# Optimization experiments

Hardware: AMD Instinct MI355X
Metric: run time of the kernel (lower is better)

## Reference

```python
import jax, jax.numpy as jnp
import numpy as np

EPS = 0.5
MU = 1.0
N_CLASS = 10
N = 131072
D = 128


def setup_inputs() -> dict:
    key = jax.random.key(0)
    k1, k2, k3 = jax.random.split(key, 3)
    Z = jax.random.normal(k1, (N, D), dtype=jnp.float32)
    labels = jax.random.randint(k2, (N,), 0, N_CLASS)
    Pi = jax.nn.one_hot(labels, N_CLASS, dtype=jnp.float32)  # [N, C] membership
    Us = jax.random.normal(k3, (N_CLASS, D, D), dtype=jnp.float32)
    return {"Z": Z, "Pi": Pi, "Us": Us}


def reference(Z, Pi, Us):
    # Z: [n, d]; forward uses Zt = Z.T of shape [d, n]
    n, d = Z.shape
    nf = jnp.asarray(n, Z.dtype)
    df = jnp.asarray(d, Z.dtype)
    I = jnp.eye(d, dtype=Z.dtype)

    # --- loss_discrimn: 0.5 * logdet(I + d/(n*eps) * Zt @ Zt.T), Zt@Zt.T = Z.T@Z ([d,d])
    gram = Z.T @ Z
    sign, logabsdet = jnp.linalg.slogdet(I + (df / (nf * EPS)) * gram)
    loss_R = 0.5 * logabsdet

    # --- loss_compress: per-class log of squared column norms of Us[j]
    trPi = Pi.sum(axis=0)                      # [C]
    col_norms_sq = (Us ** 2).sum(axis=1)       # [C, d] (norm over rows = axis 0 of Us[j])
    per_class = jnp.log1p((df / (trPi[:, None] * EPS)) * col_norms_sq).sum(axis=1)  # [C]
    loss_Rc = ((trPi / (2.0 * nf)) * per_class).sum()

    # --- reg_U: sum_j || Z.T @ diag(Pi_j) @ Z - Us[j] Us[j].T ||_F^2
    # column-scaled contraction instead of materializing n x n diag
    M = jnp.einsum('nd,nj,ne->jde', Z, Pi, Z)      # [C, d, d]
    UUt = jnp.einsum('jdk,jek->jde', Us, Us)       # [C, d, d]
    loss_reg = 0.5 * MU * ((M - UUt) ** 2).sum()

    loss_obj = loss_R - loss_Rc - loss_reg
    return (-loss_obj, loss_R, loss_Rc, loss_reg)
```

## Files before the change

kernel.cpp:

```cpp
#include <hip/hip_runtime.h>
#include <hip/hip_bf16.h>

#define DD 128
#define NCLS 10
#define CHUNK 512
#define KSTEP 32

typedef __attribute__((ext_vector_type(8))) short s16x8;
typedef __attribute__((ext_vector_type(4))) float f32x4;
typedef __attribute__((ext_vector_type(4))) unsigned int u32x4;
typedef __attribute__((ext_vector_type(8))) unsigned short u16x8;
typedef __attribute__((ext_vector_type(4))) unsigned short u16x4;

union FU { unsigned u[4]; s16x8 v; };

__device__ inline unsigned short f2bf(float x) {
  union { float f; unsigned u; } c; c.f = x;
  unsigned u = c.u;
  u += 0x7fffu + ((u >> 16) & 1u);
  return (unsigned short)(u >> 16);
}

__device__ __forceinline__ void frags4(const char* lds, int g, int m, int c0, FU* F) {
  const char* fb = lds + g * (4 * 528) + m * 4;
#pragma unroll
  for (int ft = 0; ft < 4; ft++) {
    const char* p = fb + (c0 + ft * 16) * 4;
    F[ft].u[0] = *(const unsigned*)(p);
    F[ft].u[1] = *(const unsigned*)(p + 528);
    F[ft].u[2] = *(const unsigned*)(p + 1056);
    F[ft].u[3] = *(const unsigned*)(p + 1584);
  }
}

__global__ void k_init(int* __restrict__ ws32) {
  ws32[threadIdx.x] = 0;
}

__global__ void k_label(const float* __restrict__ Pi, int N, int nbk,
                        unsigned char* __restrict__ label, int* __restrict__ meta) {
  __shared__ float pish[2560];
  __shared__ int h[NCLS];
  int t = threadIdx.x;
  if (t < NCLS) h[t] = 0;
  size_t base4 = (size_t)blockIdx.x * 640;
  size_t tot4 = (size_t)N * NCLS / 4;
  {
    const f32x4* src = (const f32x4*)Pi;
    f32x4* dst = (f32x4*)pish;
    for (int i = t; i < 640; i += 256) {
      size_t gi = base4 + i;
      f32x4 z = {0.f, 0.f, 0.f, 0.f};
      dst[i] = (gi < tot4) ? src[gi] : z;
    }
  }
  __syncthreads();
  int n = blockIdx.x * 256 + t;
  if (n < N) {
    const float* p = &pish[t * NCLS];
    float best = p[0]; int bj = 0;
#pragma unroll
    for (int j = 1; j < NCLS; j++) { float v = p[j]; if (v > best) { best = v; bj = j; } }
    label[n] = (unsigned char)bj;
    atomicAdd(&h[bj], 1);
  }
  __syncthreads();
  if (t < NCLS) {
    atomicAdd(&meta[t], h[t]);
    __threadfence();
  }
  __syncthreads();
  if (t == 0) {
    int done = atomicAdd(&meta[63], 1);
    if (done == nbk - 1) {
      int cs = 0;
      meta[10] = 0;
#pragma unroll
      for (int j = 0; j < NCLS; j++) {
        int cnt = atomicAdd(&meta[j], 0);
        int cp = (cnt + CHUNK - 1) / CHUNK;
        meta[32 + j] = cs * CHUNK;
        cs += cp;
        meta[10 + j + 1] = cs;
      }
      __threadfence();
    }
  }
}

__global__ __launch_bounds__(256) void k_pack(const float* __restrict__ Z,
                                              const float* __restrict__ Us,
                                              const unsigned char* __restrict__ label,
                                              int* __restrict__ meta,
                                              float* __restrict__ scal,
                                              unsigned short* __restrict__ packed,
                                              float* __restrict__ UUt,
                                              float nf, int nb) {
  __shared__ __align__(16) char pool[9472];
  __shared__ int h[NCLS], loff[NCLS], gbase[NCLS];
  __shared__ int slotOf[256];
  __shared__ float fred[8];
  int b = blockIdx.x, t = threadIdx.x;

  if (b < nb) {
    size_t n0 = (size_t)b * 256;
    if (t < NCLS) h[t] = 0;
    __syncthreads();
    int n = (int)n0 + t;
    int myj = 0, myr = 0;
    bool act = (n < (int)nf);
    if (act) { myj = label[n]; myr = atomicAdd(&h[myj], 1); }
    __syncthreads();
    if (t == 0) {
      int c = 0;
#pragma unroll
      for (int j = 0; j < NCLS; j++) { loff[j] = c; c += h[j]; }
    }
    __syncthreads();
    if (t < NCLS) gbase[t] = atomicAdd(&meta[32 + t], h[t]);
    __syncthreads();
    slotOf[t] = act ? (gbase[myj] + myr) : -1;
    __syncthreads();
    int rr = t >> 4, q = t & 15;
#pragma unroll 4
    for (int pass = 0; pass < 16; pass++) {
      int r = pass * 16 + rr;
      int dst = slotOf[r];
      if (dst < 0) continue;
      const float* zp = Z + (n0 + r) * DD + q * 8;
      f32x4 v0 = *(const f32x4*)zp;
      f32x4 v1 = *(const f32x4*)(zp + 4);
      u32x4 u;
      u[0] = (unsigned)f2bf(v0[0]) | ((unsigned)f2bf(v0[1]) << 16);
      u[1] = (unsigned)f2bf(v0[2]) | ((unsigned)f2bf(v0[3]) << 16);
      u[2] = (unsigned)f2bf(v1[0]) | ((unsigned)f2bf(v1[1]) << 16);
      u[3] = (unsigned)f2bf(v1[2]) | ((unsigned)f2bf(v1[3]) << 16);
      *(u32x4*)((char*)packed + (size_t)dst * 256 + q * 16) = u;
    }
  } else if (b < nb + NCLS) {
    int j = b - nb;
    int dstart = meta[10 + j] * CHUNK + meta[j];
    int dend = meta[11 + j] * CHUNK;
    int nrows = dend - dstart;
    u32x4 z = {0u, 0u, 0u, 0u};
    for (int i = t; i < nrows * 16; i += 256)
      *(u32x4*)((char*)packed + (size_t)dstart * 256 + (size_t)i * 16) = z;
  } else {
    int j = b - nb - NCLS;
    const float* U = Us + (size_t)j * 16384;
    {
      float* cs = (float*)(pool + 8448);
      float* red2 = (float*)(pool + 8960);
      int e = t & 127, half = t >> 7;
      float acc = 0.0f;
      int dd0 = half * 64;
      for (int d2 = dd0; d2 < dd0 + 64; d2++) { float v = U[d2 * 128 + e]; acc += v * v; }
      if (half == 0) cs[e] = acc;
      __syncthreads();
      float trj = (float)meta[j];
      float term = 0.0f;
      if (half == 1) {
        float tot = cs[e] + acc;
        term = log1pf((256.0f / trj) * tot);
      }
#pragma unroll
      for (int o = 32; o; o >>= 1) term += __shfl_down(term, o);
      if ((t & 63) == 0) red2[t >> 6] = term;
      __syncthreads();
      if (t == 0) atomicAdd(&scal[1], (trj / (2.0f * nf)) * (red2[2] + red2[3]));
    }
    __syncthreads();
    char* ldsY = pool;
    int l = t & 63, w = t >> 6;
    int g = l >> 4, m = l & 15;
    int d0 = (w >> 1) * 64, e0 = (w & 1) * 64;
    int sk2 = t >> 4, q = t & 15;
    f32x4 acc[4][4] = {};
    for (int ks = 0; ks < 4; ks++) {
      int k0 = ks * 32;
      __syncthreads();
      unsigned wv[8];
#pragma unroll
      for (int i = 0; i < 8; i++) {
        int c = 8 * q + i;
        wv[i] = (unsigned)f2bf(U[c * 128 + k0 + 2 * sk2])
              | ((unsigned)f2bf(U[c * 128 + k0 + 2 * sk2 + 1]) << 16);
      }
      u32x4 w0 = {wv[0], wv[1], wv[2], wv[3]};
      u32x4 w1 = {wv[4], wv[5], wv[6], wv[7]};
      *(u32x4*)(ldsY + sk2 * 528 + q * 32) = w0;
      *(u32x4*)(ldsY + sk2 * 528 + q * 32 + 16) = w1;
      __syncthreads();
      FU A[4], B[4];
      frags4(ldsY, g, m, d0, A);
      if (e0 != d0) frags4(ldsY, g, m, e0, B);
      else { for (int i = 0; i < 4; i++) B[i] = A[i]; }
#pragma unroll
      for (int dt = 0; dt < 4; dt++)
#pragma unroll
        for (int et = 0; et < 4; et++)
          acc[dt][et] = __builtin_amdgcn_mfma_f32_16x16x32_bf16(A[dt].v, B[et].v, acc[dt][et], 0, 0, 0);
    }
    float* uo = UUt + (size_t)j * 16384;
    float sq = 0.f;
#pragma unroll
    for (int dt = 0; dt < 4; dt++)
#pragma unroll
      for (int et = 0; et < 4; et++)
#pragma unroll
        for (int r = 0; r < 4; r++) {
          int row = d0 + dt * 16 + g * 4 + r;
          int col = e0 + et * 16 + m;
          float p = acc[dt][et][r];
          uo[row * 128 + col] = p;
          sq += p * p;
        }
#pragma unroll
    for (int o = 32; o; o >>= 1) sq += __shfl_down(sq, o);
    if (l == 0) fred[w] = sq;
    __syncthreads();
    if (t == 0) atomicAdd(&scal[2], fred[0] + fred[1] + fred[2] + fred[3]);
  }
}

__global__ __launch_bounds__(256, 2) void k_syrk(const unsigned short* __restrict__ packed,
                                                 const int* __restrict__ meta,
                                                 const float* __restrict__ UUt,
                                                 float* __restrict__ partial,
                                                 float* __restrict__ scal) {
  __shared__ __align__(16) char tilec[2][8448];
  __shared__ float tred[8];
  int b = blockIdx.x, t = threadIdx.x;
  if (b >= meta[20]) return;
  int l = t & 63, w = t >> 6;
  int g = l >> 4, m = l & 15;
  int d0 = (w >> 1) * 64, e0 = (w & 1) * 64;
  int sk2 = t >> 4, q = t & 15;
  size_t rowbase = (size_t)b * CHUNK;
  f32x4 acc[4][4] = {};

  auto PACKW = [&](const u16x8& a, const u16x8& bb, int buf) {
    unsigned wv[8];
#pragma unroll
    for (int i = 0; i < 8; i++)
      wv[i] = (unsigned)(unsigned short)a[i] | ((unsigned)(unsigned short)bb[i] << 16);
    u32x4 w0 = {wv[0], wv[1], wv[2], wv[3]};
    u32x4 w1 = {wv[4], wv[5], wv[6], wv[7]};
    char* tb = tilec[buf] + sk2 * 528 + q * 32;
    *(u32x4*)tb = w0;
    *(u32x4*)(tb + 16) = w1;
  };
  auto COMPUTE = [&](int buf) {
    FU A[4], B[4];
    frags4(tilec[buf], g, m, d0, A);
    if (d0 != e0) frags4(tilec[buf], g, m, e0, B);
    else { for (int i = 0; i < 4; i++) B[i] = A[i]; }
#pragma unroll
    for (int dt = 0; dt < 4; dt++)
#pragma unroll
      for (int et = 0; et < 4; et++)
        acc[dt][et] = __builtin_amdgcn_mfma_f32_16x16x32_bf16(A[dt].v, B[et].v, acc[dt][et], 0, 0, 0);
  };

  {
    const unsigned short* src = packed + rowbase * DD;
    u16x8 a = *(const u16x8*)(src + (2 * sk2) * DD + q * 8);
    u16x8 bb = *(const u16x8*)(src + (2 * sk2 + 1) * DD + q * 8);
    PACKW(a, bb, 0);
  }
  __syncthreads();
  for (int ks = 0; ks < CHUNK / KSTEP; ks++) {
    u16x8 na, nb2;
    bool more = (ks + 1 < CHUNK / KSTEP);
    if (more) {
      const unsigned short* src = packed + (rowbase + (size_t)(ks + 1) * KSTEP) * DD;
      na = *(const u16x8*)(src + (2 * sk2) * DD + q * 8);
      nb2 = *(const u16x8*)(src + (2 * sk2 + 1) * DD + q * 8);
    }
    COMPUTE(ks & 1);
    __syncthreads();
    if (more) PACKW(na, nb2, (ks + 1) & 1);
    __syncthreads();
  }

  int j = 0;
#pragma unroll
  for (int jj = 1; jj < NCLS; jj++) if (b >= meta[10 + jj]) j = jj;
  float* pb = partial + (size_t)b * 16384;
  const float* uu = UUt + (size_t)j * 16384;
  float trloc = 0.0f, dot = 0.0f;
#pragma unroll
  for (int dt = 0; dt < 4; dt++)
#pragma unroll
    for (int et = 0; et < 4; et++)
#pragma unroll
      for (int r = 0; r < 4; r++) {
        int row = d0 + dt * 16 + g * 4 + r;
        int col = e0 + et * 16 + m;
        float p = acc[dt][et][r];
        pb[row * 128 + col] = p;
        dot += p * uu[row * 128 + col];
        if (row == col) trloc += p;
      }
#pragma unroll
  for (int o = 32; o; o >>= 1) { trloc += __shfl_down(trloc, o); dot += __shfl_down(dot, o); }
  if (l == 0) { tred[w] = trloc; tred[4 + w] = dot; }
  __syncthreads();
  if (t == 0) {
    atomicAdd(&scal[0], tred[0] + tred[1] + tred[2] + tred[3]);
    atomicAdd(&scal[2], -2.0f * (tred[4] + tred[5] + tred[6] + tred[7]));
  }
}

__global__ void k_reduceE(const float* __restrict__ partial, const int* __restrict__ meta,
                          float* __restrict__ scal, float* __restrict__ E,
                          unsigned short* __restrict__ Ebf, float cf) {
  __shared__ float red[12];
  int t = threadIdx.x;
  int idx = blockIdx.x * 256 + t;
  float gsum = 0.f, sqs = 0.f;
#pragma unroll
  for (int j = 0; j < NCLS; j++) {
    int c0 = meta[10 + j], c1 = meta[11 + j];
    float s = 0.f;
#pragma unroll 4
    for (int c = c0; c < c1; c++) s += partial[(size_t)c * 16384 + idx];
    gsum += s; sqs += s * s;
  }
  float c = 1.0f + cf * scal[0] * (1.0f / 128.0f);
  float rc = 1.0f / c;
  int dg = ((idx >> 7) == (idx & 127)) ? 1 : 0;
  float e = (cf * rc) * gsum + (dg ? (rc - 1.0f) : 0.0f);
  E[idx] = e;
  Ebf[idx] = f2bf(e);
  float p1 = dg ? e : 0.0f;
  float p2 = e * e;
#pragma unroll
  for (int o = 32; o; o >>= 1) {
    p1 += __shfl_down(p1, o); p2 += __shfl_down(p2, o); sqs += __shfl_down(sqs, o);
  }
  if ((t & 63) == 0) { int wv = t >> 6; red[wv] = p1; red[4 + wv] = p2; red[8 + wv] = sqs; }
  __syncthreads();
  if (t == 0) {
    atomicAdd(&scal[3], red[0] + red[1] + red[2] + red[3]);
    atomicAdd(&scal[4], red[4] + red[5] + red[6] + red[7]);
    atomicAdd(&scal[2], red[8] + red[9] + red[10] + red[11]);
  }
}

__global__ __launch_bounds__(256) void k_final(const unsigned short* __restrict__ Ebf,
                                               const float* __restrict__ E,
                                               const float* __restrict__ scal,
                                               float* __restrict__ out, float cf) {
  __shared__ __align__(16) char ldsX[8448];
  __shared__ __align__(16) char ldsY[8448];
  __shared__ float red[4][4];
  int t = threadIdx.x;
  int l = t & 63, w = t >> 6;
  int g = l >> 4, m = l & 15;
  int d0 = (w >> 1) * 64, e0 = (w & 1) * 64;
  int sk2 = t >> 4, sq = t & 15;

  auto STAGE_X = [&](int ks) {
    int k0 = ks * 32 + 2 * sk2;
#pragma unroll
    for (int qi = 0; qi < 2; qi++) {
      int q = sq + qi * 16;
      u16x4 a = *(const u16x4*)(Ebf + k0 * 128 + q * 4);
      u16x4 bb = *(const u16x4*)(Ebf + (k0 + 1) * 128 + q * 4);
      u32x4 u;
#pragma unroll
      for (int i = 0; i < 4; i++) u[i] = (unsigned)a[i] | ((unsigned)bb[i] << 16);
      *(u32x4*)(ldsX + sk2 * 528 + q * 16) = u;
    }
  };

  f32x4 acc2[4][4] = {};
  for (int ks = 0; ks < 4; ks++) {
    __syncthreads();
    STAGE_X(ks);
    __syncthreads();
    FU A[4], B[4];
    frags4(ldsX, g, m, d0, A);
    if (e0 != d0) frags4(ldsX, g, m, e0, B);
    else { for (int i = 0; i < 4; i++) B[i] = A[i]; }
#pragma unroll
    for (int dt = 0; dt < 4; dt++)
#pragma unroll
      for (int et = 0; et < 4; et++)
        acc2[dt][et] = __builtin_amdgcn_mfma_f32_16x16x32_bf16(A[dt].v, B[et].v, acc2[dt][et], 0, 0, 0);
  }
  float t3 = 0.f, t4 = 0.f;
#pragma unroll
  for (int dt = 0; dt < 4; dt++)
#pragma unroll
    for (int et = 0; et < 4; et++)
#pragma unroll
      for (int r = 0; r < 4; r++) {
        int row = d0 + dt * 16 + g * 4 + r;
        int col = e0 + et * 16 + m;
        float p = acc2[dt][et][r];
        t3 += p * E[row * 128 + col];
        t4 += p * p;
      }

  f32x4 acc3[4][4] = {};
  for (int ks = 0; ks < 4; ks++) {
    __syncthreads();
    STAGE_X(ks);
    int dsrc = (ks < 2) ? 0 : 64;
    if (d0 == dsrc) {
      int dtb = 2 * (ks & 1);
#pragma unroll
      for (int dd = 0; dd < 2; dd++) {
        int dt = dtb + dd;
#pragma unroll
        for (int et = 0; et < 4; et++)
#pragma unroll
          for (int r = 0; r < 4; r++) {
            int lrow = dd * 16 + g * 4 + r;
            int col = e0 + et * 16 + m;
            unsigned short v = f2bf(acc2[dt][et][r]);
            *(unsigned short*)(ldsY + (lrow >> 1) * 528 + col * 4 + (lrow & 1) * 2) = v;
          }
      }
    }
    __syncthreads();
    FU A[4], B[4];
    frags4(ldsX, g, m, d0, A);
    frags4(ldsY, g, m, e0, B);
#pragma unroll
    for (int dt = 0; dt < 4; dt++)
#pragma unroll
      for (int et = 0; et < 4; et++)
        acc3[dt][et] = __builtin_amdgcn_mfma_f32_16x16x32_bf16(A[dt].v, B[et].v, acc3[dt][et], 0, 0, 0);
  }
  float t5 = 0.f, t6 = 0.f;
#pragma unroll
  for (int dt = 0; dt < 4; dt++)
#pragma unroll
    for (int et = 0; et < 4; et++)
#pragma unroll
      for (int r = 0; r < 4; r++) {
        float p = acc3[dt][et][r];
        t5 += p * acc2[dt][et][r];
        t6 += p * p;
      }

#pragma unroll
  for (int o = 32; o; o >>= 1) {
    t3 += __shfl_down(t3, o); t4 += __shfl_down(t4, o);
    t5 += __shfl_down(t5, o); t6 += __shfl_down(t6, o);
  }
  __syncthreads();
  if (l == 0) { red[w][0] = t3; red[w][1] = t4; red[w][2] = t5; red[w][3] = t6; }
  __syncthreads();
  if (t == 0) {
    float T3 = 0, T4 = 0, T5 = 0, T6 = 0;
#pragma unroll
    for (int i = 0; i < 4; i++) { T3 += red[i][0]; T4 += red[i][1]; T5 += red[i][2]; T6 += red[i][3]; }
    float c = 1.0f + cf * scal[0] * (1.0f / 128.0f);
    float t1 = scal[3], t2 = scal[4];
    float logdet = 128.0f * logf(c) + t1 - 0.5f * t2 + T3 * (1.0f / 3.0f)
                 - 0.25f * T4 + T5 * 0.2f - T6 * (1.0f / 6.0f);
    float R = 0.5f * logdet;
    float Rc = scal[1];
    float reg = 0.5f * scal[2];
    out[0] = -(R - Rc - reg);
    out[1] = R;
    out[2] = Rc;
    out[3] = reg;
  }
}

extern "C" void kernel_launch(void* const* d_in, const int* in_sizes, int n_in,
                              void* d_out, int out_size, void* d_ws, size_t ws_size,
                              hipStream_t stream) {
  const float* Z = (const float*)d_in[0];
  const float* Pi = (const float*)d_in[1];
  const float* Us = (const float*)d_in[2];
  float* out = (float*)d_out;
  int N = in_sizes[0] / DD;
  int MC = (N + CHUNK - 1) / CHUNK + NCLS;
  int NPROWS = MC * CHUNK;
  float cf = (float)DD / ((float)N * 0.5f);

  char* ws = (char*)d_ws;
  int* meta = (int*)ws;
  float* scal = (float*)(ws + 256);
  size_t off = 512;
  unsigned char* label = (unsigned char*)(ws + off);
  off += (size_t)N; off = (off + 511) & ~511ull;
  unsigned short* packed = (unsigned short*)(ws + off); off += (size_t)NPROWS * DD * 2;
  off = (off + 511) & ~511ull;
  float* UUt = (float*)(ws + off); off += (size_t)NCLS * 16384 * 4;
  float* E = (float*)(ws + off); off += (size_t)16384 * 4;
  unsigned short* Ebf = (unsigned short*)(ws + off); off += (size_t)16384 * 2;
  off = (off + 511) & ~511ull;
  float* partial = (float*)(ws + off); off += (size_t)MC * 16384 * 4;

  int nb = (N + 255) / 256;
  k_init<<<1, 128, 0, stream>>>((int*)ws);
  k_label<<<nb, 256, 0, stream>>>(Pi, N, nb, label, meta);
  k_pack<<<nb + 2 * NCLS, 256, 0, stream>>>(Z, Us, label, meta, scal, packed, UUt, (float)N, nb);
  k_syrk<<<MC, 256, 0, stream>>>(packed, meta, UUt, partial, scal);
  k_reduceE<<<64, 256, 0, stream>>>(partial, meta, scal, E, Ebf, cf);
  k_final<<<1, 256, 0, stream>>>(Ebf, E, scal, out, cf);
}
```

Before: 108.6 us.

## Replace per-block atomic slot allocation with precomputed per-block class offsets via scan

Label blocks now write per-block class histograms, and a new single-block scan kernel computes an exclusive prefix per class across blocks. The pack kernel reads those offsets directly instead of doing global atomics on shared counters and an extra round of barriers. This removes contention on ten global atomic counters and makes the packed ordering deterministic. In exchange it adds a kernel launch and a serial single-block scan over 10×512 entries.

New measurement: 115.8 us. +6.6%, slower.

```diff
diff --git a/kernel.cpp b/kernel.cpp
--- a/kernel.cpp
+++ b/kernel.cpp
@@ -38,7 +38,8 @@
 }
 
 __global__ void k_label(const float* __restrict__ Pi, int N, int nbk,
-                        unsigned char* __restrict__ label, int* __restrict__ meta) {
+                        unsigned char* __restrict__ label, int* __restrict__ meta,
+                        int* __restrict__ bh) {
   __shared__ float pish[2560];
   __shared__ int h[NCLS];
   int t = threadIdx.x;
@@ -66,6 +67,7 @@
   }
   __syncthreads();
   if (t < NCLS) {
+    bh[t * nbk + blockIdx.x] = h[t];
     atomicAdd(&meta[t], h[t]);
     __threadfence();
   }
@@ -79,11 +81,40 @@
       for (int j = 0; j < NCLS; j++) {
         int cnt = atomicAdd(&meta[j], 0);
         int cp = (cnt + CHUNK - 1) / CHUNK;
-        meta[32 + j] = cs * CHUNK;
         cs += cp;
         meta[10 + j + 1] = cs;
       }
       __threadfence();
+    }
+  }
+}
+
+__global__ __launch_bounds__(512) void k_scan(const int* __restrict__ bh,
+                                              const int* __restrict__ meta,
+                                              int* __restrict__ base, int nb) {
+  __shared__ int ws9[10];
+  int t = threadIdx.x, lane = t & 63, wid = t >> 6;
+  for (int j = 0; j < NCLS; j++) {
+    int carry = 0;
+    for (int t0 = 0; t0 < nb; t0 += 512) {
+      int idx = t0 + t;
+      int v = (idx < nb) ? bh[j * nb + idx] : 0;
+      int orig = v;
+#pragma unroll
+      for (int o = 1; o < 64; o <<= 1) { int x = __shfl_up(v, o); if (lane >= o) v += x; }
+      if (lane == 63) ws9[wid] = v;
+      __syncthreads();
+      if (t == 0) {
+        int c = 0;
+#pragma unroll
+        for (int i = 0; i < 8; i++) { int x = ws9[i]; ws9[i] = c; c += x; }
+        ws9[8] = c;
+      }
+      __syncthreads();
+      int excl = carry + ws9[wid] + v - orig;
+      if (idx < nb) base[j * nb + idx] = meta[10 + j] * CHUNK + excl;
+      carry += ws9[8];
+      __syncthreads();
     }
   }
 }
@@ -91,13 +122,14 @@
 __global__ __launch_bounds__(256) void k_pack(const float* __restrict__ Z,
                                               const float* __restrict__ Us,
                                               const unsigned char* __restrict__ label,
-                                              int* __restrict__ meta,
+                                              const int* __restrict__ meta,
+                                              const int* __restrict__ base,
                                               float* __restrict__ scal,
                                               unsigned short* __restrict__ packed,
                                               float* __restrict__ UUt,
-                                              float nf, int nb) {
+                                              float nf, int N, int nb) {
   __shared__ __align__(16) char pool[9472];
-  __shared__ int h[NCLS], loff[NCLS], gbase[NCLS];
+  __shared__ int h[NCLS];
   __shared__ int slotOf[256];
   __shared__ float fred[8];
   int b = blockIdx.x, t = threadIdx.x;
@@ -108,18 +140,9 @@
     __syncthreads();
     int n = (int)n0 + t;
     int myj = 0, myr = 0;
-    bool act = (n < (int)nf);
+    bool act = (n < N);
     if (act) { myj = label[n]; myr = atomicAdd(&h[myj], 1); }
-    __syncthreads();
-    if (t == 0) {
-      int c = 0;
-#pragma unroll
-      for (int j = 0; j < NCLS; j++) { loff[j] = c; c += h[j]; }
-    }
-    __syncthreads();
-    if (t < NCLS) gbase[t] = atomicAdd(&meta[32 + t], h[t]);
-    __syncthreads();
-    slotOf[t] = act ? (gbase[myj] + myr) : -1;
+    slotOf[t] = act ? (base[myj * nb + b] + myr) : -1;
     __syncthreads();
     int rr = t >> 4, q = t & 15;
 #pragma unroll 4
@@ -484,6 +507,7 @@
   int MC = (N + CHUNK - 1) / CHUNK + NCLS;
   int NPROWS = MC * CHUNK;
   float cf = (float)DD / ((float)N * 0.5f);
+  int nb = (N + 255) / 256;
 
   char* ws = (char*)d_ws;
   int* meta = (int*)ws;
@@ -491,6 +515,9 @@
   size_t off = 512;
   unsigned char* label = (unsigned char*)(ws + off);
   off += (size_t)N; off = (off + 511) & ~511ull;
+  int* bh = (int*)(ws + off); off += (size_t)NCLS * nb * 4;
+  int* base = (int*)(ws + off); off += (size_t)NCLS * nb * 4;
+  off = (off + 511) & ~511ull;
   unsigned short* packed = (unsigned short*)(ws + off); off += (size_t)NPROWS * DD * 2;
   off = (off + 511) & ~511ull;
   float* UUt = (float*)(ws + off); off += (size_t)NCLS * 16384 * 4;
@@ -499,10 +526,11 @@
   off = (off + 511) & ~511ull;
   float* partial = (float*)(ws + off); off += (size_t)MC * 16384 * 4;
 
-  int nb = (N + 255) / 256;
   k_init<<<1, 128, 0, stream>>>((int*)ws);
-  k_label<<<nb, 256, 0, stream>>>(Pi, N, nb, label, meta);
-  k_pack<<<nb + 2 * NCLS, 256, 0, stream>>>(Z, Us, label, meta, scal, packed, UUt, (float)N, nb);
+  k_label<<<nb, 256, 0, stream>>>(Pi, N, nb, label, meta, bh);
+  k_scan<<<1, 512, 0, stream>>>(bh, meta, base, nb);
+  k_pack<<<nb + 2 * NCLS, 256, 0, stream>>>(Z, Us, label, meta, base, scal, packed, UUt,
+                                            (float)N, N, nb);
   k_syrk<<<MC, 256, 0, stream>>>(packed, meta, UUt, partial, scal);
   k_reduceE<<<64, 256, 0, stream>>>(partial, meta, scal, E, Ebf, cf);
   k_final<<<1, 256, 0, stream>>>(Ebf, E, scal, out, cf);
```
